# Performance work log

Measured on AMD Instinct MI355X. Metric: run time of the kernel, lower is better.

## Reference

```python
import jax, jax.numpy as jnp
import numpy as np

DIM = 128
N_NODES = 50000
N_EDGES = 625000


def setup_inputs() -> dict:
    key = jax.random.key(0)
    ks = jax.random.split(key, 6)
    X = jax.random.normal(ks[0], (N_NODES, DIM), dtype=jnp.float32)
    edge_index = jax.random.randint(ks[1], (2, N_EDGES), 0, N_NODES, dtype=jnp.int64)
    # Linear params, init like torch (uniform +/- 1/sqrt(dim))
    bound = 1.0 / np.sqrt(DIM)
    msg_w = jax.random.uniform(ks[2], (DIM, DIM), minval=-bound, maxval=bound, dtype=jnp.float32)
    msg_b = jax.random.uniform(ks[3], (DIM,), minval=-bound, maxval=bound, dtype=jnp.float32)
    lin_w = jax.random.uniform(ks[4], (DIM, DIM), minval=-bound, maxval=bound, dtype=jnp.float32)
    lin_b = jax.random.uniform(ks[5], (DIM,), minval=-bound, maxval=bound, dtype=jnp.float32)
    eps = jnp.asarray(0.0, dtype=jnp.float32)
    return {"X": X, "edge_index": edge_index, "eps": eps,
            "msg_w": msg_w, "msg_b": msg_b, "lin_w": lin_w, "lin_b": lin_b}


def reference(X, edge_index, eps, msg_w, msg_b, lin_w, lin_b):
    src, dst = edge_index[0], edge_index[1]
    # msg_lin(X) then gather at dst: (E, F)
    msg = (jnp.einsum('nf,gf->ng', X, msg_w) + msg_b)[dst]
    # scatter-add messages onto src nodes: (N, F)
    agg = jax.ops.segment_sum(msg, src, num_segments=X.shape[0])
    out = (1.0 + eps) * X + agg
    out = jnp.einsum('nf,gf->ng', out, lin_w) + lin_b
    return jax.nn.relu(out)
```

## Files before the change

kernel.cpp:

```cpp
#include <hip/hip_runtime.h>
#include <hip/hip_bf16.h>

#define NN 50000
#define NE 625000
#define DIM 128

#define NBKT 782
#define NBKTP 784
#define CAP 1536
#define CHUNK 4096
#define NCHUNK ((NE + CHUNK - 1) / CHUNK)

#define XCAST_NB 6250
#define PREP_NB 65
#define SETUP_NB (NCHUNK + XCAST_NB + PREP_NB)

using fragAB = __attribute__((ext_vector_type(8))) short;
using fragC  = __attribute__((ext_vector_type(4))) float;

__device__ __forceinline__ unsigned short f2bf(float f) {
    unsigned int u = __float_as_uint(f);
    unsigned int r = u + 0x7FFFu + ((u >> 16) & 1u);
    return (unsigned short)(r >> 16);
}

__device__ __forceinline__ float bflo(unsigned v) { return __uint_as_float(v << 16); }
__device__ __forceinline__ float bfhi(unsigned v) { return __uint_as_float(v & 0xffff0000u); }

__global__ __launch_bounds__(256) void mega_setup(
    const float* __restrict__ X, const int* __restrict__ ei,
    const float* __restrict__ L, const float* __restrict__ W,
    const float* __restrict__ mb, const float* __restrict__ epsp,
    float* __restrict__ cb, unsigned short* __restrict__ Bh,
    unsigned short* __restrict__ Xbf,
    int* __restrict__ bucket_cursor, unsigned* __restrict__ staging) {
    __shared__ int cnt[NBKTP];
    __shared__ int base[NBKTP];
    __shared__ int gb[NBKTP];
    __shared__ int wsum[4];
    __shared__ unsigned staged[CHUNK];
    int blk = blockIdx.x;
    int t = threadIdx.x;

    if (blk >= NCHUNK) {
        int xb = blk - NCHUNK;
        if (xb < XCAST_NB) {
            int idx = (xb * 256 + t) * 4;
            float4 v = *(const float4*)(X + idx);
            uint2 p;
            p.x = (unsigned)f2bf(v.x) | ((unsigned)f2bf(v.y) << 16);
            p.y = (unsigned)f2bf(v.z) | ((unsigned)f2bf(v.w) << 16);
            *(uint2*)(Xbf + idx) = p;
        } else {
            int idx = (xb - XCAST_NB) * 256 + t;
            float scale = 1.0f + *epsp;
            if (idx < DIM * DIM) {
                int o = idx >> 7, g = idx & 127;
                float s = 0.f;
                for (int f = 0; f < DIM; f++) s += L[o * DIM + f] * W[f * DIM + g];
                Bh[o * 256 + 128 + g] = f2bf(s);
                Bh[o * 256 + g] = f2bf(L[o * DIM + g] * scale);
            } else if (idx < DIM * DIM + DIM) {
                int o = idx - DIM * DIM;
                float s = 0.f;
                for (int f = 0; f < DIM; f++) s += L[o * DIM + f] * mb[f];
                cb[o] = s;
            }
        }
        return;
    }

    int e0 = blk * CHUNK;
    int nthis = NE - e0; if (nthis > CHUNK) nthis = CHUNK;

    for (int i = t; i < NBKTP; i += 256) cnt[i] = 0;
    __syncthreads();

    unsigned pk[CHUNK / 256];
#pragma unroll
    for (int i = 0; i < CHUNK / 256; i++) {
        int e = e0 + i * 256 + t;
        if (e < NE) {
            int s = ei[e];
            int d = ei[NE + e];
            unsigned b = (unsigned)s >> 6;
            pk[i] = (b << 22) | ((unsigned)(s & 63) << 16) | (unsigned)d;
            atomicAdd(&cnt[b], 1);
        } else pk[i] = 0xFFFFFFFFu;
    }
    __syncthreads();

    int myb = t * 4;
    int s0 = 0;
    if (myb < NBKTP) s0 = cnt[myb] + cnt[myb + 1] + cnt[myb + 2] + cnt[myb + 3];
    int lane = t & 63, w = t >> 6;
    int v = s0;
#pragma unroll
    for (int off = 1; off < 64; off <<= 1) {
        int u = __shfl_up(v, off);
        if (lane >= off) v += u;
    }
    if (lane == 63) wsum[w] = v;
    __syncthreads();
    int add = 0;
#pragma unroll
    for (int i = 0; i < 4; i++)
        if (i < w) add += wsum[i];
    int run = v + add - s0;
    if (myb < NBKTP) {
        for (int i = 0; i < 4; i++) {
            int b = myb + i;
            base[b] = run;
            int c = cnt[b];
            gb[b] = (b < NBKT && c > 0) ? atomicAdd(&bucket_cursor[b], c) : 0;
            run += c;
        }
    }
    __syncthreads();
    if (myb < NBKTP) {
        for (int i = 0; i < 4; i++) cnt[myb + i] = base[myb + i];
    }
    __syncthreads();

#pragma unroll
    for (int i = 0; i < CHUNK / 256; i++) {
        if (pk[i] != 0xFFFFFFFFu) {
            unsigned b = pk[i] >> 22;
            int pos = atomicAdd(&cnt[b], 1);
            staged[pos] = pk[i];
        }
    }
    __syncthreads();

    for (int idx = t; idx < nthis; idx += 256) {
        unsigned p = staged[idx];
        unsigned b = p >> 22;
        int pos = gb[b] + (idx - base[b]);
        if (pos >= 0 && pos < CAP) staging[(size_t)b * CAP + pos] = p;
    }
}

__global__ __launch_bounds__(512, 4) void gather_gemm(
    const int* __restrict__ bucket_cursor, const unsigned* __restrict__ staging,
    const unsigned short* __restrict__ Xbf, const unsigned short* __restrict__ Bh,
    const float* __restrict__ cb, const float* __restrict__ lin_b,
    float* __restrict__ out) {
    __shared__ unsigned rec[CAP];
    __shared__ unsigned sorted_[CAP];
    __shared__ int hcnt[64];
    __shared__ int hbase[64];
    __shared__ int cur[64];
    __shared__ unsigned short As[64 * 264];
    int t = threadIdx.x;
    int b = blockIdx.x;
    int cnt_b = bucket_cursor[b];
    if (cnt_b > CAP) cnt_b = CAP;

    if (t < 64) hcnt[t] = 0;
#pragma unroll
    for (int it = 0; it < 2; it++) {
        int idx = t + it * 512;
        int row = idx >> 4, c = idx & 15;
        int node = b * 64 + row;
        if (node >= NN) node = NN - 1;
        uint4 vx = *(const uint4*)(Xbf + (size_t)node * 128 + c * 8);
        *(uint4*)(As + row * 264 + c * 8) = vx;
    }
    __syncthreads();
    for (int i = t; i < cnt_b; i += 512) {
        unsigned r = staging[(size_t)b * CAP + i];
        rec[i] = r;
        atomicAdd(&hcnt[(r >> 16) & 63], 1);
    }
    __syncthreads();
    if (t < 64) {
        int c = hcnt[t];
        int v = c;
#pragma unroll
        for (int off = 1; off < 64; off <<= 1) {
            int u = __shfl_up(v, off);
            if (t >= off) v += u;
        }
        int ex = v - c;
        hbase[t] = ex;
        cur[t] = ex;
    }
    __syncthreads();
    for (int i = t; i < cnt_b; i += 512) {
        unsigned r = rec[i];
        int pos = atomicAdd(&cur[(r >> 16) & 63], 1);
        sorted_[pos] = r;
    }
    __syncthreads();

    int wave = t >> 6, lane = t & 63;
    int l32 = lane & 31, half = lane >> 5;
    const uint2* __restrict__ X2 = (const uint2*)Xbf;
    for (int ni = 0; ni < 8; ni++) {
        int local = wave * 8 + ni;
        int node = b * 64 + local;
        if (node >= NN) continue;
        int start = hbase[local];
        int cnt = hcnt[local];
        float a0 = 0.f, a1 = 0.f, a2 = 0.f, a3 = 0.f;
        int pairs = cnt >> 1;
        int j = 0;
        for (; j + 8 <= pairs; j += 8) {
            int d[8];
#pragma unroll
            for (int i = 0; i < 8; i++)
                d[i] = (int)(sorted_[start + 2 * (j + i) + half] & 0xFFFFu);
            uint2 v[8];
#pragma unroll
            for (int i = 0; i < 8; i++) v[i] = X2[(size_t)d[i] * 32 + l32];
#pragma unroll
            for (int i = 0; i < 8; i++) {
                a0 += bflo(v[i].x);
                a1 += bfhi(v[i].x);
                a2 += bflo(v[i].y);
                a3 += bfhi(v[i].y);
            }
        }
        for (; j < pairs; j++) {
            int d = (int)(sorted_[start + 2 * j + half] & 0xFFFFu);
            uint2 v = X2[(size_t)d * 32 + l32];
            a0 += bflo(v.x);
            a1 += bfhi(v.x);
            a2 += bflo(v.y);
            a3 += bfhi(v.y);
        }
        if ((cnt & 1) && half == 0) {
            int d = (int)(sorted_[start + cnt - 1] & 0xFFFFu);
            uint2 v = X2[(size_t)d * 32 + l32];
            a0 += bflo(v.x);
            a1 += bfhi(v.x);
            a2 += bflo(v.y);
            a3 += bfhi(v.y);
        }
        a0 += __shfl_xor(a0, 32);
        a1 += __shfl_xor(a1, 32);
        a2 += __shfl_xor(a2, 32);
        a3 += __shfl_xor(a3, 32);
        if (half == 0) {
            uint2 p;
            p.x = (unsigned)f2bf(a0) | ((unsigned)f2bf(a1) << 16);
            p.y = (unsigned)f2bf(a2) | ((unsigned)f2bf(a3) << 16);
            *(uint2*)(As + local * 264 + 128 + l32 * 4) = p;
        }
    }
    __syncthreads();

    int m16 = lane & 15;
    int quad = lane >> 4;
    int waveM = (wave & 3) * 16;
    int waveN = (wave >> 2) * 64;

    fragC acc[4];
#pragma unroll
    for (int j = 0; j < 4; j++) acc[j] = (fragC){0.f, 0.f, 0.f, 0.f};

#pragma unroll
    for (int kc = 0; kc < 8; kc++) {
        fragAB a = *(const fragAB*)(As + (waveM + m16) * 264 + kc * 32 + quad * 8);
#pragma unroll
        for (int j = 0; j < 4; j++) {
            fragAB bf = *(const fragAB*)(Bh + (size_t)(waveN + j * 16 + m16) * 256 + kc * 32 + quad * 8);
            acc[j] = __builtin_amdgcn_mfma_f32_16x16x32_bf16(a, bf, acc[j], 0, 0, 0);
        }
    }

#pragma unroll
    for (int j = 0; j < 4; j++) {
        int col = waveN + j * 16 + m16;
        float cbc = cb[col];
        float lbc = lin_b[col];
        int lr = waveM + quad * 4;
#pragma unroll
        for (int r = 0; r < 4; r++) {
            int row = lr + r;
            int node = b * 64 + row;
            if (node < NN) {
                float dg = (float)hcnt[row];
                float v = acc[j][r] + dg * cbc + lbc;
                out[(size_t)node * 128 + col] = fmaxf(v, 0.f);
            }
        }
    }
}

extern "C" void kernel_launch(void* const* d_in, const int* in_sizes, int n_in,
                              void* d_out, int out_size, void* d_ws, size_t ws_size,
                              hipStream_t stream) {
    const float* X = (const float*)d_in[0];
    const int* ei = (const int*)d_in[1];
    const float* epsp = (const float*)d_in[2];
    const float* msg_w = (const float*)d_in[3];
    const float* msg_b = (const float*)d_in[4];
    const float* lin_w = (const float*)d_in[5];
    const float* lin_b = (const float*)d_in[6];
    float* out = (float*)d_out;

    int* bucket_cursor = (int*)d_ws;
    unsigned* staging = (unsigned*)(bucket_cursor + 800);
    float* cb = (float*)(staging + (size_t)NBKT * CAP);
    unsigned short* Bh = (unsigned short*)(cb + DIM);
    unsigned short* Xbf = Bh + 128 * 256;

    hipMemsetAsync(bucket_cursor, 0, NBKTP * sizeof(int), stream);

    mega_setup<<<SETUP_NB, 256, 0, stream>>>(X, ei, lin_w, msg_w, msg_b, epsp, cb, Bh, Xbf,
                                             bucket_cursor, staging);
    gather_gemm<<<NBKT, 512, 0, stream>>>(bucket_cursor, staging, Xbf, Bh, cb, lin_b, out);
}
```

Before: 181.5 us.

## Shrink bucket capacity, raise occupancy, and widen gather to 16-byte loads

Bucket capacity drops to 1024 and the rec shared buffer is removed, with staged records kept in registers instead. This cuts LDS use so launch bounds can request 8 blocks per CU instead of 4. The X tile and record loads are issued up front and the LDS writes happen later, overlapping global load latency with the histogram. The neighbor gather now uses uint4 loads with four quarter-wave groups, which needs an extra shuffle reduction step. Buckets holding more than 1024 edges would now drop records, which is a correctness risk if the degree distribution is skewed.

```diff
diff --git a/kernel.cpp b/kernel.cpp
--- a/kernel.cpp
+++ b/kernel.cpp
@@ -7,7 +7,7 @@
 
 #define NBKT 782
 #define NBKTP 784
-#define CAP 1536
+#define CAP 1024
 #define CHUNK 4096
 #define NCHUNK ((NE + CHUNK - 1) / CHUNK)
 
@@ -140,12 +140,11 @@
     }
 }
 
-__global__ __launch_bounds__(512, 4) void gather_gemm(
+__global__ __launch_bounds__(512, 8) void gather_gemm(
     const int* __restrict__ bucket_cursor, const unsigned* __restrict__ staging,
     const unsigned short* __restrict__ Xbf, const unsigned short* __restrict__ Bh,
     const float* __restrict__ cb, const float* __restrict__ lin_b,
     float* __restrict__ out) {
-    __shared__ unsigned rec[CAP];
     __shared__ unsigned sorted_[CAP];
     __shared__ int hcnt[64];
     __shared__ int hbase[64];
@@ -156,22 +155,21 @@
     int cnt_b = bucket_cursor[b];
     if (cnt_b > CAP) cnt_b = CAP;
 
+    int xrow0 = t >> 4, xc0 = t & 15;
+    int xrow1 = xrow0 + 32;
+    int xnode0 = b * 64 + xrow0; if (xnode0 >= NN) xnode0 = NN - 1;
+    int xnode1 = b * 64 + xrow1; if (xnode1 >= NN) xnode1 = NN - 1;
+    uint4 xv0 = *(const uint4*)(Xbf + (size_t)xnode0 * 128 + xc0 * 8);
+    uint4 xv1 = *(const uint4*)(Xbf + (size_t)xnode1 * 128 + xc0 * 8);
+
+    unsigned r0 = 0xFFFFFFFFu, r1 = 0xFFFFFFFFu;
+    if (t < cnt_b) r0 = staging[(size_t)b * CAP + t];
+    if (t + 512 < cnt_b) r1 = staging[(size_t)b * CAP + t + 512];
+
     if (t < 64) hcnt[t] = 0;
-#pragma unroll
-    for (int it = 0; it < 2; it++) {
-        int idx = t + it * 512;
-        int row = idx >> 4, c = idx & 15;
-        int node = b * 64 + row;
-        if (node >= NN) node = NN - 1;
-        uint4 vx = *(const uint4*)(Xbf + (size_t)node * 128 + c * 8);
-        *(uint4*)(As + row * 264 + c * 8) = vx;
-    }
-    __syncthreads();
-    for (int i = t; i < cnt_b; i += 512) {
-        unsigned r = staging[(size_t)b * CAP + i];
-        rec[i] = r;
-        atomicAdd(&hcnt[(r >> 16) & 63], 1);
-    }
+    __syncthreads();
+    if (r0 != 0xFFFFFFFFu) atomicAdd(&hcnt[(r0 >> 16) & 63], 1);
+    if (r1 != 0xFFFFFFFFu) atomicAdd(&hcnt[(r1 >> 16) & 63], 1);
     __syncthreads();
     if (t < 64) {
         int c = hcnt[t];
@@ -186,16 +184,21 @@
         cur[t] = ex;
     }
     __syncthreads();
-    for (int i = t; i < cnt_b; i += 512) {
-        unsigned r = rec[i];
-        int pos = atomicAdd(&cur[(r >> 16) & 63], 1);
-        sorted_[pos] = r;
-    }
+    if (r0 != 0xFFFFFFFFu) {
+        int pos = atomicAdd(&cur[(r0 >> 16) & 63], 1);
+        sorted_[pos] = r0;
+    }
+    if (r1 != 0xFFFFFFFFu) {
+        int pos = atomicAdd(&cur[(r1 >> 16) & 63], 1);
+        sorted_[pos] = r1;
+    }
+    *(uint4*)(As + xrow0 * 264 + xc0 * 8) = xv0;
+    *(uint4*)(As + xrow1 * 264 + xc0 * 8) = xv1;
     __syncthreads();
 
     int wave = t >> 6, lane = t & 63;
-    int l32 = lane & 31, half = lane >> 5;
-    const uint2* __restrict__ X2 = (const uint2*)Xbf;
+    int q = lane >> 4, l16 = lane & 15;
+    const uint4* __restrict__ X4 = (const uint4*)Xbf;
     for (int ni = 0; ni < 8; ni++) {
         int local = wave * 8 + ni;
         int node = b * 64 + local;
@@ -203,49 +206,45 @@
         int start = hbase[local];
         int cnt = hcnt[local];
         float a0 = 0.f, a1 = 0.f, a2 = 0.f, a3 = 0.f;
-        int pairs = cnt >> 1;
-        int j = 0;
-        for (; j + 8 <= pairs; j += 8) {
-            int d[8];
-#pragma unroll
-            for (int i = 0; i < 8; i++)
-                d[i] = (int)(sorted_[start + 2 * (j + i) + half] & 0xFFFFu);
-            uint2 v[8];
-#pragma unroll
-            for (int i = 0; i < 8; i++) v[i] = X2[(size_t)d[i] * 32 + l32];
-#pragma unroll
-            for (int i = 0; i < 8; i++) {
-                a0 += bflo(v[i].x);
-                a1 += bfhi(v[i].x);
-                a2 += bflo(v[i].y);
-                a3 += bfhi(v[i].y);
-            }
-        }
-        for (; j < pairs; j++) {
-            int d = (int)(sorted_[start + 2 * j + half] & 0xFFFFu);
-            uint2 v = X2[(size_t)d * 32 + l32];
-            a0 += bflo(v.x);
-            a1 += bfhi(v.x);
-            a2 += bflo(v.y);
-            a3 += bfhi(v.y);
-        }
-        if ((cnt & 1) && half == 0) {
-            int d = (int)(sorted_[start + cnt - 1] & 0xFFFFu);
-            uint2 v = X2[(size_t)d * 32 + l32];
-            a0 += bflo(v.x);
-            a1 += bfhi(v.x);
-            a2 += bflo(v.y);
-            a3 += bfhi(v.y);
-        }
-        a0 += __shfl_xor(a0, 32);
-        a1 += __shfl_xor(a1, 32);
-        a2 += __shfl_xor(a2, 32);
-        a3 += __shfl_xor(a3, 32);
-        if (half == 0) {
-            uint2 p;
+        float a4 = 0.f, a5 = 0.f, a6 = 0.f, a7 = 0.f;
+        int j = q;
+        for (; j + 4 < cnt; j += 8) {
+            int d0 = (int)(sorted_[start + j] & 0xFFFFu);
+            int d1 = (int)(sorted_[start + j + 4] & 0xFFFFu);
+            uint4 v0 = X4[(size_t)d0 * 16 + l16];
+            uint4 v1 = X4[(size_t)d1 * 16 + l16];
+            a0 += bflo(v0.x); a1 += bfhi(v0.x);
+            a2 += bflo(v0.y); a3 += bfhi(v0.y);
+            a4 += bflo(v0.z); a5 += bfhi(v0.z);
+            a6 += bflo(v0.w); a7 += bfhi(v0.w);
+            a0 += bflo(v1.x); a1 += bfhi(v1.x);
+            a2 += bflo(v1.y); a3 += bfhi(v1.y);
+            a4 += bflo(v1.z); a5 += bfhi(v1.z);
+            a6 += bflo(v1.w); a7 += bfhi(v1.w);
+        }
+        if (j < cnt) {
+            int d0 = (int)(sorted_[start + j] & 0xFFFFu);
+            uint4 v0 = X4[(size_t)d0 * 16 + l16];
+            a0 += bflo(v0.x); a1 += bfhi(v0.x);
+            a2 += bflo(v0.y); a3 += bfhi(v0.y);
+            a4 += bflo(v0.z); a5 += bfhi(v0.z);
+            a6 += bflo(v0.w); a7 += bfhi(v0.w);
+        }
+        a0 += __shfl_xor(a0, 16); a1 += __shfl_xor(a1, 16);
+        a2 += __shfl_xor(a2, 16); a3 += __shfl_xor(a3, 16);
+        a4 += __shfl_xor(a4, 16); a5 += __shfl_xor(a5, 16);
+        a6 += __shfl_xor(a6, 16); a7 += __shfl_xor(a7, 16);
+        a0 += __shfl_xor(a0, 32); a1 += __shfl_xor(a1, 32);
+        a2 += __shfl_xor(a2, 32); a3 += __shfl_xor(a3, 32);
+        a4 += __shfl_xor(a4, 32); a5 += __shfl_xor(a5, 32);
+        a6 += __shfl_xor(a6, 32); a7 += __shfl_xor(a7, 32);
+        if (q == 0) {
+            uint4 p;
             p.x = (unsigned)f2bf(a0) | ((unsigned)f2bf(a1) << 16);
             p.y = (unsigned)f2bf(a2) | ((unsigned)f2bf(a3) << 16);
-            *(uint2*)(As + local * 264 + 128 + l32 * 4) = p;
+            p.z = (unsigned)f2bf(a4) | ((unsigned)f2bf(a5) << 16);
+            p.w = (unsigned)f2bf(a6) | ((unsigned)f2bf(a7) << 16);
+            *(uint4*)(As + local * 264 + 128 + l16 * 8) = p;
         }
     }
     __syncthreads();
```

New measurement: 159.0 us. 1.14x faster.

## Balance gather across waves with LDS float atomics instead of per-node reduction

Applied to the files above, without the earlier changes.

The gather phase now splits the bucket's edge list evenly across the eight waves, with edges sorted by source-node partition, and accumulates into a 64x128 fp32 LDS tile using atomic adds. This replaces the old scheme, where each wave owned eight destination nodes. The self-feature half of the A operand is now read directly from global memory during the MFMA loop rather than staged in LDS. A zeroed dummy row is added past the end of Xbf for padding. This removes load imbalance from skewed node degrees at the cost of many LDS atomics and a larger shared footprint, and occupancy is raised in the launch bounds.

```diff
diff --git a/kernel.cpp b/kernel.cpp
--- a/kernel.cpp
+++ b/kernel.cpp
@@ -140,113 +140,93 @@
     }
 }
 
-__global__ __launch_bounds__(512, 4) void gather_gemm(
+__global__ __launch_bounds__(512, 8) void gather_gemm(
     const int* __restrict__ bucket_cursor, const unsigned* __restrict__ staging,
     const unsigned short* __restrict__ Xbf, const unsigned short* __restrict__ Bh,
     const float* __restrict__ cb, const float* __restrict__ lin_b,
     float* __restrict__ out) {
-    __shared__ unsigned rec[CAP];
+    __shared__ float Acc[64 * 128];
     __shared__ unsigned sorted_[CAP];
     __shared__ int hcnt[64];
-    __shared__ int hbase[64];
-    __shared__ int cur[64];
-    __shared__ unsigned short As[64 * 264];
+    __shared__ int pcnt[8];
+    __shared__ int pbase[8];
+    __shared__ int pcur[8];
+    unsigned short* As = (unsigned short*)Acc;
+
     int t = threadIdx.x;
     int b = blockIdx.x;
     int cnt_b = bucket_cursor[b];
     if (cnt_b > CAP) cnt_b = CAP;
 
+    unsigned r0 = 0xFFFFFFFFu, r1 = 0xFFFFFFFFu, r2 = 0xFFFFFFFFu;
+    if (t < cnt_b) r0 = staging[(size_t)b * CAP + t];
+    if (t + 512 < cnt_b) r1 = staging[(size_t)b * CAP + t + 512];
+    if (t + 1024 < cnt_b) r2 = staging[(size_t)b * CAP + t + 1024];
+
+    {
+        uint4 z = (uint4){0, 0, 0, 0};
+        uint4* az = (uint4*)Acc + t * 4;
+        az[0] = z; az[1] = z; az[2] = z; az[3] = z;
+    }
     if (t < 64) hcnt[t] = 0;
-#pragma unroll
-    for (int it = 0; it < 2; it++) {
-        int idx = t + it * 512;
-        int row = idx >> 4, c = idx & 15;
-        int node = b * 64 + row;
-        if (node >= NN) node = NN - 1;
-        uint4 vx = *(const uint4*)(Xbf + (size_t)node * 128 + c * 8);
-        *(uint4*)(As + row * 264 + c * 8) = vx;
-    }
-    __syncthreads();
-    for (int i = t; i < cnt_b; i += 512) {
-        unsigned r = staging[(size_t)b * CAP + i];
-        rec[i] = r;
-        atomicAdd(&hcnt[(r >> 16) & 63], 1);
-    }
-    __syncthreads();
-    if (t < 64) {
-        int c = hcnt[t];
-        int v = c;
-#pragma unroll
-        for (int off = 1; off < 64; off <<= 1) {
-            int u = __shfl_up(v, off);
-            if (t >= off) v += u;
-        }
-        int ex = v - c;
-        hbase[t] = ex;
-        cur[t] = ex;
-    }
-    __syncthreads();
-    for (int i = t; i < cnt_b; i += 512) {
-        unsigned r = rec[i];
-        int pos = atomicAdd(&cur[(r >> 16) & 63], 1);
-        sorted_[pos] = r;
-    }
+    if (t < 8) pcnt[t] = 0;
+    __syncthreads();
+    if (r0 != 0xFFFFFFFFu) { atomicAdd(&hcnt[(r0 >> 16) & 63], 1); atomicAdd(&pcnt[(r0 & 0xFFFFu) >> 13], 1); }
+    if (r1 != 0xFFFFFFFFu) { atomicAdd(&hcnt[(r1 >> 16) & 63], 1); atomicAdd(&pcnt[(r1 & 0xFFFFu) >> 13], 1); }
+    if (r2 != 0xFFFFFFFFu) { atomicAdd(&hcnt[(r2 >> 16) & 63], 1); atomicAdd(&pcnt[(r2 & 0xFFFFu) >> 13], 1); }
+    __syncthreads();
+    if (t == 0) {
+        int run = 0;
+#pragma unroll
+        for (int i = 0; i < 8; i++) { pbase[i] = run; pcur[i] = run; run += pcnt[i]; }
+    }
+    __syncthreads();
+    if (r0 != 0xFFFFFFFFu) { int p = atomicAdd(&pcur[(r0 & 0xFFFFu) >> 13], 1); sorted_[p] = r0; }
+    if (r1 != 0xFFFFFFFFu) { int p = atomicAdd(&pcur[(r1 & 0xFFFFu) >> 13], 1); sorted_[p] = r1; }
+    if (r2 != 0xFFFFFFFFu) { int p = atomicAdd(&pcur[(r2 & 0xFFFFu) >> 13], 1); sorted_[p] = r2; }
     __syncthreads();
 
     int wave = t >> 6, lane = t & 63;
-    int l32 = lane & 31, half = lane >> 5;
-    const uint2* __restrict__ X2 = (const uint2*)Xbf;
-    for (int ni = 0; ni < 8; ni++) {
-        int local = wave * 8 + ni;
-        int node = b * 64 + local;
-        if (node >= NN) continue;
-        int start = hbase[local];
-        int cnt = hcnt[local];
-        float a0 = 0.f, a1 = 0.f, a2 = 0.f, a3 = 0.f;
-        int pairs = cnt >> 1;
-        int j = 0;
-        for (; j + 8 <= pairs; j += 8) {
-            int d[8];
-#pragma unroll
-            for (int i = 0; i < 8; i++)
-                d[i] = (int)(sorted_[start + 2 * (j + i) + half] & 0xFFFFu);
-            uint2 v[8];
-#pragma unroll
-            for (int i = 0; i < 8; i++) v[i] = X2[(size_t)d[i] * 32 + l32];
-#pragma unroll
-            for (int i = 0; i < 8; i++) {
-                a0 += bflo(v[i].x);
-                a1 += bfhi(v[i].x);
-                a2 += bflo(v[i].y);
-                a3 += bfhi(v[i].y);
+    {
+        int lo = (cnt_b * wave) >> 3;
+        int hi = (cnt_b * (wave + 1)) >> 3;
+        const unsigned DUMMY = (unsigned)NN;
+        int feat = lane << 1;
+        for (int e = lo; e < hi; e += 8) {
+            unsigned rr[8], vv[8];
+#pragma unroll
+            for (int k = 0; k < 8; k++) {
+                int j = e + k;
+                rr[k] = (j < hi) ? sorted_[j] : DUMMY;
             }
-        }
-        for (; j < pairs; j++) {
-            int d = (int)(sorted_[start + 2 * j + half] & 0xFFFFu);
-            uint2 v = X2[(size_t)d * 32 + l32];
-            a0 += bflo(v.x);
-            a1 += bfhi(v.x);
-            a2 += bflo(v.y);
-            a3 += bfhi(v.y);
-        }
-        if ((cnt & 1) && half == 0) {
-            int d = (int)(sorted_[start + cnt - 1] & 0xFFFFu);
-            uint2 v = X2[(size_t)d * 32 + l32];
-            a0 += bflo(v.x);
-            a1 += bfhi(v.x);
-            a2 += bflo(v.y);
-            a3 += bfhi(v.y);
-        }
-        a0 += __shfl_xor(a0, 32);
-        a1 += __shfl_xor(a1, 32);
-        a2 += __shfl_xor(a2, 32);
-        a3 += __shfl_xor(a3, 32);
-        if (half == 0) {
-            uint2 p;
-            p.x = (unsigned)f2bf(a0) | ((unsigned)f2bf(a1) << 16);
-            p.y = (unsigned)f2bf(a2) | ((unsigned)f2bf(a3) << 16);
-            *(uint2*)(As + local * 264 + 128 + l32 * 4) = p;
-        }
+#pragma unroll
+            for (int k = 0; k < 8; k++)
+                vv[k] = *(const unsigned*)(Xbf + (size_t)(rr[k] & 0xFFFFu) * 128 + feat);
+#pragma unroll
+            for (int k = 0; k < 8; k++) {
+                int l = (int)((rr[k] >> 16) & 63);
+                float* ap = &Acc[l * 128 + feat];
+                atomicAdd(ap, bflo(vv[k]));
+                atomicAdd(ap + 1, bfhi(vv[k]));
+            }
+        }
+    }
+    __syncthreads();
+
+    {
+        float va[16];
+        const float* src = Acc + t * 16;
+#pragma unroll
+        for (int i = 0; i < 16; i++) va[i] = src[i];
+        __syncthreads();
+        int r = t >> 3, c0 = (t & 7) * 16;
+        unsigned pk[8];
+#pragma unroll
+        for (int i = 0; i < 8; i++)
+            pk[i] = (unsigned)f2bf(va[2 * i]) | ((unsigned)f2bf(va[2 * i + 1]) << 16);
+        uint4* dst = (uint4*)(As + r * 136 + c0);
+        dst[0] = (uint4){pk[0], pk[1], pk[2], pk[3]};
+        dst[1] = (uint4){pk[4], pk[5], pk[6], pk[7]};
     }
     __syncthreads();
 
@@ -259,9 +239,20 @@
 #pragma unroll
     for (int j = 0; j < 4; j++) acc[j] = (fragC){0.f, 0.f, 0.f, 0.f};
 
-#pragma unroll
-    for (int kc = 0; kc < 8; kc++) {
-        fragAB a = *(const fragAB*)(As + (waveM + m16) * 264 + kc * 32 + quad * 8);
+    int xr = b * 64 + waveM + m16;
+    if (xr >= NN) xr = NN;
+#pragma unroll
+    for (int kc = 0; kc < 4; kc++) {
+        fragAB a = *(const fragAB*)(Xbf + (size_t)xr * 128 + kc * 32 + quad * 8);
+#pragma unroll
+        for (int j = 0; j < 4; j++) {
+            fragAB bf = *(const fragAB*)(Bh + (size_t)(waveN + j * 16 + m16) * 256 + kc * 32 + quad * 8);
+            acc[j] = __builtin_amdgcn_mfma_f32_16x16x32_bf16(a, bf, acc[j], 0, 0, 0);
+        }
+    }
+#pragma unroll
+    for (int kc = 4; kc < 8; kc++) {
+        fragAB a = *(const fragAB*)(As + (waveM + m16) * 136 + (kc - 4) * 32 + quad * 8);
 #pragma unroll
         for (int j = 0; j < 4; j++) {
             fragAB bf = *(const fragAB*)(Bh + (size_t)(waveN + j * 16 + m16) * 256 + kc * 32 + quad * 8);
@@ -301,12 +292,13 @@
     float* out = (float*)d_out;
 
     int* bucket_cursor = (int*)d_ws;
-    unsigned* staging = (unsigned*)(bucket_cursor + 800);
+    unsigned* staging = (unsigned*)(bucket_cursor + NBKTP);
     float* cb = (float*)(staging + (size_t)NBKT * CAP);
     unsigned short* Bh = (unsigned short*)(cb + DIM);
     unsigned short* Xbf = Bh + 128 * 256;
 
     hipMemsetAsync(bucket_cursor, 0, NBKTP * sizeof(int), stream);
+    hipMemsetAsync(Xbf + (size_t)NN * 128, 0, 128 * sizeof(unsigned short), stream);
 
     mega_setup<<<SETUP_NB, 256, 0, stream>>>(X, ei, lin_w, msg_w, msg_b, epsp, cb, Bh, Xbf,
                                              bucket_cursor, staging);
```

New measurement: 685.8 us. 278% more time.
